# Performance work log

Measured on AMD Instinct MI355X. Metric: run time of the kernel, lower is better.

Reference implementation:

```python
import jax, jax.numpy as jnp
import numpy as np

B, S, D_IN, D_OUT, H = 2, 2048, 1024, 1024, 16
HD = D_OUT // H  # head dim = 64


def setup_inputs() -> dict:
    key = jax.random.key(0)
    ks = jax.random.split(key, 9)
    s_in = 1.0 / np.sqrt(D_IN)
    s_out = 1.0 / np.sqrt(D_OUT)
    return {
        "X": jax.random.normal(ks[0], (B, S, D_IN), dtype=jnp.float32),
        "Wq": jax.random.uniform(ks[1], (D_OUT, D_IN), jnp.float32, -s_in, s_in),
        "bq": jax.random.uniform(ks[2], (D_OUT,), jnp.float32, -s_in, s_in),
        "Wk": jax.random.uniform(ks[3], (D_OUT, D_IN), jnp.float32, -s_in, s_in),
        "bk": jax.random.uniform(ks[4], (D_OUT,), jnp.float32, -s_in, s_in),
        "Wv": jax.random.uniform(ks[5], (D_OUT, D_IN), jnp.float32, -s_in, s_in),
        "bv": jax.random.uniform(ks[6], (D_OUT,), jnp.float32, -s_in, s_in),
        "Wo": jax.random.uniform(ks[7], (D_OUT, D_OUT), jnp.float32, -s_out, s_out),
        "bo": jax.random.uniform(ks[8], (D_OUT,), jnp.float32, -s_out, s_out),
    }


def reference(X, Wq, bq, Wk, bk, Wv, bv, Wo, bo):
    scale = jnp.asarray(HD ** 0.5, X.dtype)  # self.dim = sqrt(head_dim)
    q = X @ Wq.T + bq  # [B,S,D_OUT]
    k = X @ Wk.T + bk
    v = X @ Wv.T + bv
    # split heads: b s (h d) -> b h s d
    q = q.reshape(B, S, H, HD).transpose(0, 2, 1, 3)
    k = k.reshape(B, S, H, HD).transpose(0, 2, 1, 3)
    v = v.reshape(B, S, H, HD).transpose(0, 2, 1, 3)
    scores = jnp.einsum('bhsd,bhtd->bhst', q, k) / scale  # [B,H,S,S]
    causal = jnp.triu(jnp.ones((S, S), dtype=bool), k=1)
    scores = jnp.where(causal, -jnp.inf, scores)
    weights = jax.nn.softmax(scores, axis=-1)
    out = jnp.einsum('bhst,bhtd->bhsd', weights, v)  # [B,H,S,HD]
    out = out.transpose(0, 2, 1, 3).reshape(B, S, D_OUT)  # b h s d -> b s (h d)
    return out @ Wo.T + bo
```

## Files before the change

### kernel.cpp

```cpp
#include <hip/hip_runtime.h>
#include <hip/hip_bf16.h>

typedef __bf16 bf16_t;
typedef __bf16 bf16x8 __attribute__((ext_vector_type(8)));
typedef float  f32x4  __attribute__((ext_vector_type(4)));
typedef unsigned short ushort_t;

#define MFMA16(a, b, c) __builtin_amdgcn_mfma_f32_16x16x32_bf16((a), (b), (c), 0, 0, 0)
#define GLDS16(g, l) __builtin_amdgcn_global_load_lds( \
    (const __attribute__((address_space(1))) unsigned int*)(g), \
    (__attribute__((address_space(3))) unsigned int*)(l), 16, 0, 0)

#define WAITCNT_VM(n)  (0x0F70 | (n))
#define WAITCNT_LGKM0  0xC07F

#define MEMFENCE asm volatile("" ::: "memory")

#define SWZ(r) ((((r) >> 1) ^ ((r) >> 3)) & 3)

#define QSCALE 0.18033688f

__global__ __launch_bounds__(256) void cvt_all(
    const void* __restrict__ X,  const void* __restrict__ W0, const void* __restrict__ W1,
    const void* __restrict__ W2, const void* __restrict__ W3,
    const void* __restrict__ c0, const void* __restrict__ c1,
    const void* __restrict__ c2, const void* __restrict__ c3,
    bf16_t* __restrict__ Xb, bf16_t* __restrict__ Wb, float* __restrict__ biasF,
    int* __restrict__ flag)
{
    const int tid  = threadIdx.x;
    const int lane = tid & 63;
    const ushort_t u = ((const ushort_t*)X)[2 * lane];
    const int e = (u >> 7) & 0xFF;
    const int f = (__ballot(e >= 0xA0) != 0ull) ? 1 : 0;

    const int bid = blockIdx.x;
    if (bid >= 4096) {
        if (bid == 4096 && tid == 0) *flag = f;
        const int idx = ((bid - 4096) * 256 + tid) * 8;
        const int w = idx >> 10, off = idx & 1023;
        const void* src = (w == 0) ? c0 : (w == 1) ? c1 : (w == 2) ? c2 : c3;
        #pragma unroll
        for (int r = 0; r < 8; ++r)
            biasF[idx + r] = f ? ((const float*)src)[off + r]
                               : (float)((const bf16_t*)src)[off + r];
        return;
    }

    const long long i = (long long)bid * 2048 + tid * 8;
    const void* src;
    bf16_t* dst;
    long long off;
    if (i < 4194304) { src = X; dst = Xb; off = i; }
    else {
        const int w = (int)((i - 4194304) >> 20);
        off = (i - 4194304) & 1048575;
        src = (w == 0) ? W0 : (w == 1) ? W1 : (w == 2) ? W2 : W3;
        dst = Wb + (size_t)w * 1048576;
    }
    if (f) {
        const float* s = (const float*)src + off;
        const float4 a = *(const float4*)(s);
        const float4 b = *(const float4*)(s + 4);
        bf16x8 o;
        o[0] = (bf16_t)a.x; o[1] = (bf16_t)a.y; o[2] = (bf16_t)a.z; o[3] = (bf16_t)a.w;
        o[4] = (bf16_t)b.x; o[5] = (bf16_t)b.y; o[6] = (bf16_t)b.z; o[7] = (bf16_t)b.w;
        *(bf16x8*)(dst + off) = o;
    } else {
        *(bf16x8*)(dst + off) = *(const bf16x8*)((const bf16_t*)src + off);
    }
}

__global__ __launch_bounds__(512, 2) void gemm_qkv(
    const bf16_t* __restrict__ A,
    const bf16_t* __restrict__ Wst,
    const float* __restrict__ biasAll,
    bf16_t* __restrict__ C, bf16_t* __restrict__ Vt)
{
    __shared__ bf16_t Ash[4][256 * 32];
    __shared__ bf16_t Bsh[4][192 * 32];

    const int tid  = threadIdx.x;
    const int wid  = tid >> 6;
    const int lane = tid & 63;
    const int g    = lane >> 4;
    const int c    = lane & 15;

    const int m0 = blockIdx.x * 256;
    const int n0 = blockIdx.y * 192;

    const int srow = lane >> 2;
    const int sblk = (lane & 3) ^ ((lane >> 3) & 3);
    const bf16_t* Ag  = A   + (size_t)(m0 + wid * 32 + srow) * 1024 + sblk * 8;
    const bf16_t* Wg0 = Wst + (size_t)(n0 + wid * 16 + srow) * 1024 + sblk * 8;
    const bf16_t* Wg1 = Wst + (size_t)(n0 + 128 + wid * 16 + srow) * 1024 + sblk * 8;

    const int waveM = (wid >> 2) * 128;
    const int waveN = (wid & 3) * 48;
    const int fblk  = (g ^ ((c >> 1) & 3)) * 8;

    f32x4 acc[8][3] = {};

    auto stage = [&](int H) {
        const int buf = H & 3;
        GLDS16(Ag + H * 32,                      &Ash[buf][(wid * 32) * 32]);
        GLDS16(Ag + (size_t)16 * 1024 + H * 32,  &Ash[buf][(wid * 32 + 16) * 32]);
        GLDS16(Wg0 + H * 32,                     &Bsh[buf][(wid * 16) * 32]);
        if (wid < 4)
            GLDS16(Wg1 + H * 32,                 &Bsh[buf][(128 + wid * 16) * 32]);
    };

    stage(0); stage(1); stage(2);
    if (wid < 4) __builtin_amdgcn_s_waitcnt(WAITCNT_VM(8));
    else         __builtin_amdgcn_s_waitcnt(WAITCNT_VM(6));
    __builtin_amdgcn_s_barrier();
    MEMFENCE;

    #pragma unroll 4
    for (int H = 0; H < 32; ++H) {
        const int buf = H & 3;
        const bf16_t* As = Ash[buf];
        const bf16_t* Bs = Bsh[buf];

        bf16x8 bfr[3], af[8];
        #pragma unroll
        for (int j = 0; j < 3; ++j)
            bfr[j] = *(const bf16x8*)(&Bs[(waveN + j * 16 + c) * 32 + fblk]);
        #pragma unroll
        for (int i = 0; i < 8; ++i)
            af[i] = *(const bf16x8*)(&As[(waveM + i * 16 + c) * 32 + fblk]);

        if (H < 29) stage(H + 3);

        __builtin_amdgcn_s_setprio(1);
        #pragma unroll
        for (int i = 0; i < 8; ++i)
            #pragma unroll
            for (int j = 0; j < 3; ++j)
                acc[i][j] = MFMA16(af[i], bfr[j], acc[i][j]);
        __builtin_amdgcn_s_setprio(0);

        MEMFENCE;
        __builtin_amdgcn_s_waitcnt(WAITCNT_LGKM0);
        if (H < 29) {
            if (wid < 4) __builtin_amdgcn_s_waitcnt(WAITCNT_VM(8));
            else         __builtin_amdgcn_s_waitcnt(WAITCNT_VM(6));
        } else if (H == 29) {
            if (wid < 4) __builtin_amdgcn_s_waitcnt(WAITCNT_VM(4));
            else         __builtin_amdgcn_s_waitcnt(WAITCNT_VM(3));
        } else if (H == 30) {
            __builtin_amdgcn_s_waitcnt(WAITCNT_VM(0));
        }
        __builtin_amdgcn_s_barrier();
        MEMFENCE;
    }

    #pragma unroll
    for (int j = 0; j < 3; ++j) {
        const int cg0 = n0 + waveN + j * 16;
        const int col = cg0 + c;
        const float bv = biasAll[col];
        if (cg0 >= 2048) {
            const int hcol = col - 2048;
            const int h = hcol >> 6, d = hcol & 63;
            #pragma unroll
            for (int i = 0; i < 8; ++i) {
                const int row = m0 + waveM + i * 16 + g * 4;
                const int bb = row >> 11, s = row & 2047;
                bf16_t pk[4];
                #pragma unroll
                for (int r = 0; r < 4; ++r) pk[r] = (bf16_t)(acc[i][j][r] + bv);
                *(uint2*)(&Vt[(((size_t)bb * 16 + h) * 64 + d) * 2048 + s]) = *(uint2*)pk;
            }
        } else {
            const float os = (cg0 < 1024) ? QSCALE : 1.0f;
            #pragma unroll
            for (int i = 0; i < 8; ++i) {
                const int row = m0 + waveM + i * 16 + g * 4;
                #pragma unroll
                for (int r = 0; r < 4; ++r)
                    C[(size_t)(row + r) * 3072 + col] = (bf16_t)((acc[i][j][r] + bv) * os);
            }
        }
    }
}

template<int TM>
__global__ __launch_bounds__(256, 3) void gemm_nt(
    const bf16_t* __restrict__ A,
    const bf16_t* __restrict__ W0,
    const float* __restrict__ b0,
    void* __restrict__ C, int ldc,
    const int* __restrict__ flag, int is_out)
{
    constexpr int MI = TM / 32;
    __shared__ bf16_t Ash[2][TM * 32];
    __shared__ bf16_t Bsh[2][128 * 32];

    const int f32out = is_out ? *flag : 0;

    const int tid  = threadIdx.x;
    const int wid  = tid >> 6;
    const int lane = tid & 63;
    const int g    = lane >> 4;
    const int c    = lane & 15;

    const int m0  = blockIdx.x * TM;
    const int n0  = blockIdx.y * 128;
    const bf16_t* W  = W0;
    const float*  bs = b0;
    const int nw = n0 & 1023;

    const int srow = lane >> 2;
    const int sblk = (lane & 3) ^ ((lane >> 3) & 3);
    const bf16_t* Ag = A + (size_t)(m0 + wid * (TM / 4) + srow) * 1024 + sblk * 8;
    const bf16_t* Wg = W + (size_t)(nw + wid * 32 + srow) * 1024 + sblk * 8;

    const int waveM = (wid >> 1) * (TM / 2);
    const int waveN = (wid & 1) * 64;

    f32x4 acc[MI][4] = {};
    const int fblk = (g ^ ((c >> 1) & 3)) * 8;

    auto stage = [&](int t) {
        const int k0 = t * 32;
        const int buf = t & 1;
        bf16_t* As = &Ash[buf][(wid * (TM / 4)) * 32];
        bf16_t* Bs = &Bsh[buf][(wid * 32) * 32];
        GLDS16(Ag + k0, As);
        if (TM == 128) GLDS16(Ag + (size_t)16 * 1024 + k0, As + 16 * 32);
        GLDS16(Wg + k0, Bs);
        GLDS16(Wg + (size_t)16 * 1024 + k0, Bs + 16 * 32);
    };

    stage(0);
    __builtin_amdgcn_s_waitcnt(WAITCNT_VM(0));
    __builtin_amdgcn_s_barrier();
    MEMFENCE;

    #pragma unroll 2
    for (int k = 0; k < 32; ++k) {
        const int cur = k & 1;
        bf16x8 af[MI], bfr[4];
        #pragma unroll
        for (int i = 0; i < MI; ++i)
            af[i] = *(const bf16x8*)(&Ash[cur][(waveM + i * 16 + c) * 32 + fblk]);
        #pragma unroll
        for (int j = 0; j < 4; ++j)
            bfr[j] = *(const bf16x8*)(&Bsh[cur][(waveN + j * 16 + c) * 32 + fblk]);

        if (k < 31) stage(k + 1);

        __builtin_amdgcn_s_setprio(1);
        #pragma unroll
        for (int i = 0; i < MI; ++i)
            #pragma unroll
            for (int j = 0; j < 4; ++j)
                acc[i][j] = MFMA16(af[i], bfr[j], acc[i][j]);
        __builtin_amdgcn_s_setprio(0);

        MEMFENCE;
        __builtin_amdgcn_s_waitcnt(WAITCNT_LGKM0);
        if (k < 31) __builtin_amdgcn_s_waitcnt(WAITCNT_VM(0));
        __builtin_amdgcn_s_barrier();
        MEMFENCE;
    }

    #pragma unroll
    for (int j = 0; j < 4; ++j) {
        const int col = n0 + waveN + j * 16 + c;
        const float bv = bs[col & 1023];
        #pragma unroll
        for (int i = 0; i < MI; ++i) {
            const int row = m0 + waveM + i * 16 + g * 4;
            #pragma unroll
            for (int r = 0; r < 4; ++r) {
                const float val = acc[i][j][r] + bv;
                const size_t idx = (size_t)(row + r) * ldc + col;
                if (f32out) ((float*)C)[idx] = val;
                else        ((bf16_t*)C)[idx] = (bf16_t)val;
            }
        }
    }
}

__global__ __launch_bounds__(256, 4) void attn_kernel(
    const bf16_t* __restrict__ QKV, const bf16_t* __restrict__ Vt,
    bf16_t* __restrict__ O)
{
    __shared__ bf16_t Ksh[2][64][32];
    __shared__ bf16_t Vsh[2][64][32];
    __shared__ bf16_t Psh[4][2][16][32];

    const int tid  = threadIdx.x;
    const int wid  = tid >> 6;
    const int lane = tid & 63;
    const int g    = lane >> 4;
    const int c    = lane & 15;

    const int bh = blockIdx.y;
    const int b  = bh >> 4, h = bh & 15;
    const int qt = (bh < 16) ? blockIdx.x : (31 - blockIdx.x);
    const int q0 = qt * 64;
    const int nt = qt + 1;

    bf16x8 aq[2];
    {
        const bf16_t* qp = QKV + (size_t)(b * 2048 + q0 + wid * 16 + c) * 3072 + h * 64;
        aq[0] = *(const bf16x8*)(qp + g * 8);
        aq[1] = *(const bf16x8*)(qp + 32 + g * 8);
    }

    float li[4] = {};
    f32x4 o[4]  = {};

    const int sr = tid >> 2;
    const int j4 = tid & 3;
    const bf16_t* Kg = QKV + (size_t)(b * 2048 + sr) * 3072 + 1024 + h * 64 + j4 * 8;
    const bf16_t* Vg = Vt + ((size_t)bh * 64 + sr) * 2048 + j4 * 8;

    const int sp = (j4 ^ SWZ(sr)) * 8;
    bf16_t* kd0 = &Ksh[0][sr][sp];
    bf16_t* kd1 = &Ksh[1][sr][sp];
    bf16_t* vd0 = &Vsh[0][sr][sp];
    bf16_t* vd1 = &Vsh[1][sr][sp];

    uint4 kr0 = *(const uint4*)(Kg);
    uint4 kr1 = *(const uint4*)(Kg + 32);
    uint4 vr0 = *(const uint4*)(Vg);
    uint4 vr1 = *(const uint4*)(Vg + 32);

    for (int jt = 0; jt < nt; ++jt) {
        *(uint4*)kd0 = kr0;
        *(uint4*)kd1 = kr1;
        *(uint4*)vd0 = vr0;
        *(uint4*)vd1 = vr1;
        __syncthreads();

        if (jt + 1 < nt) {
            const size_t ko = (size_t)(jt + 1) * 64 * 3072;
            kr0 = *(const uint4*)(Kg + ko);
            kr1 = *(const uint4*)(Kg + ko + 32);
            vr0 = *(const uint4*)(Vg + (jt + 1) * 64);
            vr1 = *(const uint4*)(Vg + (jt + 1) * 64 + 32);
        }

        f32x4 s[4] = {};
        __builtin_amdgcn_s_setprio(1);
        #pragma unroll
        for (int n = 0; n < 4; ++n)
            #pragma unroll
            for (int kb = 0; kb < 2; ++kb) {
                const int row = n * 16 + c;
                const bf16x8 kf = *(const bf16x8*)(&Ksh[kb][row][(g ^ SWZ(row)) * 8]);
                s[n] = MFMA16(aq[kb], kf, s[n]);
            }
        __builtin_amdgcn_s_setprio(0);

        if (jt == nt - 1) {
            const int j0 = jt * 64;
            const int qrow = q0 + wid * 16 + g * 4;
            #pragma unroll
            for (int n = 0; n < 4; ++n)
                #pragma unroll
                for (int r = 0; r < 4; ++r)
                    if (j0 + n * 16 + c > qrow + r) s[n][r] = -1e30f;
        }

        #pragma unroll
        for (int n = 0; n < 4; ++n)
            #pragma unroll
            for (int r = 0; r < 4; ++r) {
                const float p = __builtin_amdgcn_exp2f(s[n][r]);
                li[r] += p;
                const int q  = g * 4 + r;
                const int gg = 2 * n + (c >> 3);
                Psh[wid][gg >> 2][q][((gg & 3) ^ SWZ(q)) * 8 + (c & 7)] = (bf16_t)p;
            }
        __builtin_amdgcn_wave_barrier();

        __builtin_amdgcn_s_setprio(1);
        #pragma unroll
        for (int kb = 0; kb < 2; ++kb) {
            const bf16x8 ap = *(const bf16x8*)(&Psh[wid][kb][c][(g ^ SWZ(c)) * 8]);
            #pragma unroll
            for (int d = 0; d < 4; ++d) {
                const int row = d * 16 + c;
                const bf16x8 vf = *(const bf16x8*)(&Vsh[kb][row][(g ^ SWZ(row)) * 8]);
                o[d] = MFMA16(ap, vf, o[d]);
            }
        }
        __builtin_amdgcn_s_setprio(0);
        __syncthreads();
    }

    #pragma unroll
    for (int off = 1; off < 16; off <<= 1)
        #pragma unroll
        for (int r = 0; r < 4; ++r)
            li[r] += __shfl_xor(li[r], off, 64);

    const int orow = b * 2048 + q0 + wid * 16 + g * 4;
    #pragma unroll
    for (int r = 0; r < 4; ++r) {
        const float inv = 1.0f / li[r];
        #pragma unroll
        for (int d = 0; d < 4; ++d)
            O[(size_t)(orow + r) * 1024 + h * 64 + d * 16 + c] = (bf16_t)(o[d][r] * inv);
    }
}

extern "C" void kernel_launch(void* const* d_in, const int* in_sizes, int n_in,
                              void* d_out, int out_size, void* d_ws, size_t ws_size,
                              hipStream_t stream)
{
    const void* X  = d_in[0];
    const void* Wq = d_in[1];  const void* bq = d_in[2];
    const void* Wk = d_in[3];  const void* bk = d_in[4];
    const void* Wv = d_in[5];  const void* bv = d_in[6];
    const void* Wo = d_in[7];  const void* bo = d_in[8];

    int*    flag  = (int*)d_ws;
    float*  biasF = (float*)((char*)d_ws + 16);
    bf16_t* Xb    = (bf16_t*)((char*)d_ws + 16 + 16384);
    bf16_t* Wb    = Xb  + (size_t)4096 * 1024;
    bf16_t* QKV   = Wb  + (size_t)4 * 1024 * 1024;
    bf16_t* Vt    = QKV + (size_t)4096 * 3072;
    bf16_t* Ao    = Vt  + (size_t)4096 * 1024;

    const size_t MW = (size_t)1024 * 1024;

    cvt_all<<<4098, 256, 0, stream>>>(X, Wq, Wk, Wv, Wo, bq, bk, bv, bo,
                                      Xb, Wb, biasF, flag);

    gemm_qkv<<<dim3(16, 16), 512, 0, stream>>>(Xb, Wb, biasF, QKV, Vt);
    attn_kernel<<<dim3(32, 32), 256, 0, stream>>>(QKV, Vt, Ao);
    gemm_nt<64><<<dim3(64, 8), 256, 0, stream>>>(
        Ao, Wb + 3 * MW, biasF + 3072, d_out, 1024, flag, 1);
}
```

Before: 194.3 us.

## Transpose attention MFMA operands so each lane owns a query row

Swaps the A/B operands of both MFMAs so scores and outputs come out transposed: each lane holds one query row with four consecutive key/dim values. This lets P be written to LDS as packed 8-byte stores and read back as two 8-byte loads. The row-sum then needs only two cross-lane shuffles instead of sixteen, and the output is written as packed 4-element stores. The P buffer layout and its swizzle change to match, which adds some risk of LDS bank conflicts.

```diff
diff --git a/kernel.cpp b/kernel.cpp
--- a/kernel.cpp
+++ b/kernel.cpp
@@ -290,7 +290,7 @@
 {
     __shared__ bf16_t Ksh[2][64][32];
     __shared__ bf16_t Vsh[2][64][32];
-    __shared__ bf16_t Psh[4][2][16][32];
+    __shared__ bf16_t Psh[4][16][72];
 
     const int tid  = threadIdx.x;
     const int wid  = tid >> 6;
@@ -311,8 +311,8 @@
         aq[1] = *(const bf16x8*)(qp + 32 + g * 8);
     }
 
-    float li[4] = {};
-    f32x4 o[4]  = {};
+    float li = 0.0f;
+    f32x4 o2[4] = {};
 
     const int sr = tid >> 2;
     const int j4 = tid & 3;
@@ -329,6 +329,8 @@
     uint4 kr1 = *(const uint4*)(Kg + 32);
     uint4 vr0 = *(const uint4*)(Vg);
     uint4 vr1 = *(const uint4*)(Vg + 32);
+
+    const int qg = q0 + wid * 16 + c;
 
     for (int jt = 0; jt < nt; ++jt) {
         *(uint4*)kd0 = kr0;
@@ -353,60 +355,71 @@
             for (int kb = 0; kb < 2; ++kb) {
                 const int row = n * 16 + c;
                 const bf16x8 kf = *(const bf16x8*)(&Ksh[kb][row][(g ^ SWZ(row)) * 8]);
-                s[n] = MFMA16(aq[kb], kf, s[n]);
+                s[n] = MFMA16(kf, aq[kb], s[n]);
             }
         __builtin_amdgcn_s_setprio(0);
 
         if (jt == nt - 1) {
             const int j0 = jt * 64;
-            const int qrow = q0 + wid * 16 + g * 4;
             #pragma unroll
             for (int n = 0; n < 4; ++n)
                 #pragma unroll
                 for (int r = 0; r < 4; ++r)
-                    if (j0 + n * 16 + c > qrow + r) s[n][r] = -1e30f;
-        }
-
-        #pragma unroll
-        for (int n = 0; n < 4; ++n)
-            #pragma unroll
-            for (int r = 0; r < 4; ++r) {
-                const float p = __builtin_amdgcn_exp2f(s[n][r]);
-                li[r] += p;
-                const int q  = g * 4 + r;
-                const int gg = 2 * n + (c >> 3);
-                Psh[wid][gg >> 2][q][((gg & 3) ^ SWZ(q)) * 8 + (c & 7)] = (bf16_t)p;
+                    if (j0 + n * 16 + g * 4 + r > qg) s[n][r] = -1e30f;
+        }
+
+        #pragma unroll
+        for (int n = 0; n < 4; ++n) {
+            const float p0 = __builtin_amdgcn_exp2f(s[n][0]);
+            const float p1 = __builtin_amdgcn_exp2f(s[n][1]);
+            const float p2 = __builtin_amdgcn_exp2f(s[n][2]);
+            const float p3 = __builtin_amdgcn_exp2f(s[n][3]);
+            li += (p0 + p1) + (p2 + p3);
+            union { bf16_t h[4]; uint2 u; } pk;
+            pk.h[0] = (bf16_t)p0; pk.h[1] = (bf16_t)p1;
+            pk.h[2] = (bf16_t)p2; pk.h[3] = (bf16_t)p3;
+            const int pw = ((n ^ (c >> 2)) << 2) + (g ^ (c & 3));
+            *(uint2*)(&Psh[wid][c][pw * 4]) = pk.u;
+        }
+        __builtin_amdgcn_wave_barrier();
+
+        bf16x8 pb[2];
+        #pragma unroll
+        for (int kb = 0; kb < 2; ++kb) {
+            const int n0  = 2 * kb + (g >> 1);
+            const int gs  = (g & 1) * 2;
+            const int base = ((n0 ^ (c >> 2)) << 2);
+            const uint2 w0 = *(const uint2*)(&Psh[wid][c][(base + (gs ^ (c & 3))) * 4]);
+            const uint2 w1 = *(const uint2*)(&Psh[wid][c][(base + ((gs + 1) ^ (c & 3))) * 4]);
+            union { uint4 u; bf16x8 v; } cvt;
+            cvt.u.x = w0.x; cvt.u.y = w0.y; cvt.u.z = w1.x; cvt.u.w = w1.y;
+            pb[kb] = cvt.v;
+        }
+
+        __builtin_amdgcn_s_setprio(1);
+        #pragma unroll
+        for (int kb = 0; kb < 2; ++kb)
+            #pragma unroll
+            for (int dt = 0; dt < 4; ++dt) {
+                const int row = dt * 16 + c;
+                const bf16x8 vf = *(const bf16x8*)(&Vsh[kb][row][(g ^ SWZ(row)) * 8]);
+                o2[dt] = MFMA16(vf, pb[kb], o2[dt]);
             }
-        __builtin_amdgcn_wave_barrier();
-
-        __builtin_amdgcn_s_setprio(1);
-        #pragma unroll
-        for (int kb = 0; kb < 2; ++kb) {
-            const bf16x8 ap = *(const bf16x8*)(&Psh[wid][kb][c][(g ^ SWZ(c)) * 8]);
-            #pragma unroll
-            for (int d = 0; d < 4; ++d) {
-                const int row = d * 16 + c;
-                const bf16x8 vf = *(const bf16x8*)(&Vsh[kb][row][(g ^ SWZ(row)) * 8]);
-                o[d] = MFMA16(ap, vf, o[d]);
-            }
-        }
         __builtin_amdgcn_s_setprio(0);
         __syncthreads();
     }
 
+    li += __shfl_xor(li, 16, 64);
+    li += __shfl_xor(li, 32, 64);
+    const float inv = 1.0f / li;
+
+    const size_t orow = (size_t)(b * 2048 + q0 + wid * 16 + c);
     #pragma unroll
-    for (int off = 1; off < 16; off <<= 1)
-        #pragma unroll
-        for (int r = 0; r < 4; ++r)
-            li[r] += __shfl_xor(li[r], off, 64);
-
-    const int orow = b * 2048 + q0 + wid * 16 + g * 4;
-    #pragma unroll
-    for (int r = 0; r < 4; ++r) {
-        const float inv = 1.0f / li[r];
-        #pragma unroll
-        for (int d = 0; d < 4; ++d)
-            O[(size_t)(orow + r) * 1024 + h * 64 + d * 16 + c] = (bf16_t)(o[d][r] * inv);
+    for (int dt = 0; dt < 4; ++dt) {
+        union { bf16_t h[4]; uint2 u; } pk;
+        #pragma unroll
+        for (int r = 0; r < 4; ++r) pk.h[r] = (bf16_t)(o2[dt][r] * inv);
+        *(uint2*)(&O[orow * 1024 + h * 64 + dt * 16 + g * 4]) = pk.u;
     }
 }
 
```

After: 194.8 us. About the same (+0.3%).
